# Performance work log

Measured on AMD Instinct MI355X. Metric: run time of the kernel, lower is better.

The kernel has to match this reference:

```python
import jax, jax.numpy as jnp
import numpy as np

N = 33554432  # 32M elements, 128 MB fp32

def setup_inputs() -> dict:
    key = jax.random.key(0)
    inp = jax.random.uniform(key, (N,), dtype=jnp.float32)
    return {"inp": inp}

def reference(inp) -> jnp.ndarray:
    # Faithful to the original: exp(x) / sum(exp(inp)) with NO max-subtraction
    # (the torch module computes the unstabilized softmax).
    e = jnp.exp(inp)
    return e / jnp.sum(e)
```

## Files before the change

### kernel.cpp

```cpp
#include <hip/hip_runtime.h>


#define BLOCK 256
#define RGRID 2048
#define SGRID 2048

typedef float vfloat4 __attribute__((ext_vector_type(4)));

__global__ __launch_bounds__(BLOCK) void softmax_reduce(
    const float* __restrict__ inp, float* __restrict__ partials, int n4) {
  const vfloat4* __restrict__ in4 = (const vfloat4*)inp;
  int tid = blockIdx.x * BLOCK + threadIdx.x;
  int stride = gridDim.x * BLOCK;

  float s0 = 0.0f, s1 = 0.0f;
  int i = tid;
  for (; i + stride < n4; i += 2 * stride) {
    vfloat4 a = in4[i];
    vfloat4 b = in4[i + stride];
    s0 += __expf(a.x) + __expf(a.y) + __expf(a.z) + __expf(a.w);
    s1 += __expf(b.x) + __expf(b.y) + __expf(b.z) + __expf(b.w);
  }
  for (; i < n4; i += stride) {
    vfloat4 a = in4[i];
    s0 += __expf(a.x) + __expf(a.y) + __expf(a.z) + __expf(a.w);
  }
  float s = s0 + s1;

  #pragma unroll
  for (int off = 32; off > 0; off >>= 1)
    s += __shfl_down(s, off, 64);

  __shared__ float wsum[BLOCK / 64];
  if ((threadIdx.x & 63) == 0) wsum[threadIdx.x >> 6] = s;
  __syncthreads();
  if (threadIdx.x == 0)
    partials[blockIdx.x] = wsum[0] + wsum[1] + wsum[2] + wsum[3];
}

__global__ __launch_bounds__(BLOCK) void softmax_scale(
    const float* __restrict__ inp, float* __restrict__ out,
    const float* __restrict__ partials, int n4) {
  float t = 0.0f;
  #pragma unroll
  for (int i = 0; i < RGRID / BLOCK; ++i)
    t += partials[i * BLOCK + threadIdx.x];

  #pragma unroll
  for (int off = 32; off > 0; off >>= 1)
    t += __shfl_down(t, off, 64);

  __shared__ float wsum[BLOCK / 64];
  if ((threadIdx.x & 63) == 0) wsum[threadIdx.x >> 6] = t;
  __syncthreads();
  float r = 1.0f / (wsum[0] + wsum[1] + wsum[2] + wsum[3]);

  const vfloat4* __restrict__ in4 = (const vfloat4*)inp;
  vfloat4* __restrict__ out4 = (vfloat4*)out;
  int tid = blockIdx.x * BLOCK + threadIdx.x;
  int stride = gridDim.x * BLOCK;

  int i = tid;
  for (; i + stride < n4; i += 2 * stride) {
    vfloat4 a = in4[i];
    vfloat4 b = in4[i + stride];
    vfloat4 oa, ob;
    oa.x = __expf(a.x) * r; oa.y = __expf(a.y) * r;
    oa.z = __expf(a.z) * r; oa.w = __expf(a.w) * r;
    ob.x = __expf(b.x) * r; ob.y = __expf(b.y) * r;
    ob.z = __expf(b.z) * r; ob.w = __expf(b.w) * r;
    __builtin_nontemporal_store(oa, &out4[i]);
    __builtin_nontemporal_store(ob, &out4[i + stride]);
  }
  for (; i < n4; i += stride) {
    vfloat4 a = in4[i];
    vfloat4 oa;
    oa.x = __expf(a.x) * r; oa.y = __expf(a.y) * r;
    oa.z = __expf(a.z) * r; oa.w = __expf(a.w) * r;
    __builtin_nontemporal_store(oa, &out4[i]);
  }
}

extern "C" void kernel_launch(void* const* d_in, const int* in_sizes, int n_in,
                              void* d_out, int out_size, void* d_ws, size_t ws_size,
                              hipStream_t stream) {
  const float* inp = (const float*)d_in[0];
  float* out = (float*)d_out;
  float* partials = (float*)d_ws;
  int n = in_sizes[0];
  int n4 = n >> 2;

  softmax_reduce<<<RGRID, BLOCK, 0, stream>>>(inp, partials, n4);
  softmax_scale<<<SGRID, BLOCK, 0, stream>>>(inp, out, partials, n4);
}
```

Baseline: 246.6 us.

## Store exp values in first pass and rescale output in place

The first kernel now writes exp(x) to the output buffer while accumulating partial sums, and reads the input with nontemporal loads. The second kernel reads that stored buffer back and multiplies by the reciprocal of the total, instead of re-reading the input and recomputing exp. This removes the second round of exp work, but it raises memory traffic from two reads and one write to two reads and two writes of the full array. Whether it pays off depends on the output buffer staying cached between the two passes.

```diff
diff --git a/kernel.cpp b/kernel.cpp
--- a/kernel.cpp
+++ b/kernel.cpp
@@ -2,28 +2,40 @@
 
 
 #define BLOCK 256
-#define RGRID 2048
-#define SGRID 2048
+#define GRID 2048
 
 typedef float vfloat4 __attribute__((ext_vector_type(4)));
 
-__global__ __launch_bounds__(BLOCK) void softmax_reduce(
-    const float* __restrict__ inp, float* __restrict__ partials, int n4) {
+__global__ __launch_bounds__(BLOCK) void softmax_pass1(
+    const float* __restrict__ inp, float* __restrict__ out,
+    float* __restrict__ partials, int n4) {
   const vfloat4* __restrict__ in4 = (const vfloat4*)inp;
-  int tid = blockIdx.x * BLOCK + threadIdx.x;
-  int stride = gridDim.x * BLOCK;
+  vfloat4* __restrict__ out4 = (vfloat4*)out;
+  const int tid = blockIdx.x * BLOCK + threadIdx.x;
+  const int stride = GRID * BLOCK;
 
   float s0 = 0.0f, s1 = 0.0f;
   int i = tid;
   for (; i + stride < n4; i += 2 * stride) {
-    vfloat4 a = in4[i];
-    vfloat4 b = in4[i + stride];
-    s0 += __expf(a.x) + __expf(a.y) + __expf(a.z) + __expf(a.w);
-    s1 += __expf(b.x) + __expf(b.y) + __expf(b.z) + __expf(b.w);
+    vfloat4 a = __builtin_nontemporal_load(&in4[i]);
+    vfloat4 b = __builtin_nontemporal_load(&in4[i + stride]);
+    vfloat4 ea, eb;
+    ea.x = __expf(a.x); ea.y = __expf(a.y);
+    ea.z = __expf(a.z); ea.w = __expf(a.w);
+    eb.x = __expf(b.x); eb.y = __expf(b.y);
+    eb.z = __expf(b.z); eb.w = __expf(b.w);
+    out4[i] = ea;
+    out4[i + stride] = eb;
+    s0 += ea.x + ea.y + ea.z + ea.w;
+    s1 += eb.x + eb.y + eb.z + eb.w;
   }
   for (; i < n4; i += stride) {
-    vfloat4 a = in4[i];
-    s0 += __expf(a.x) + __expf(a.y) + __expf(a.z) + __expf(a.w);
+    vfloat4 a = __builtin_nontemporal_load(&in4[i]);
+    vfloat4 ea;
+    ea.x = __expf(a.x); ea.y = __expf(a.y);
+    ea.z = __expf(a.z); ea.w = __expf(a.w);
+    out4[i] = ea;
+    s0 += ea.x + ea.y + ea.z + ea.w;
   }
   float s = s0 + s1;
 
@@ -38,13 +50,12 @@
     partials[blockIdx.x] = wsum[0] + wsum[1] + wsum[2] + wsum[3];
 }
 
-__global__ __launch_bounds__(BLOCK) void softmax_scale(
-    const float* __restrict__ inp, float* __restrict__ out,
-    const float* __restrict__ partials, int n4) {
+__global__ __launch_bounds__(BLOCK) void softmax_pass2(
+    float* __restrict__ out, const float* __restrict__ partials, int n4) {
   float t = 0.0f;
   #pragma unroll
-  for (int i = 0; i < RGRID / BLOCK; ++i)
-    t += partials[i * BLOCK + threadIdx.x];
+  for (int k = 0; k < GRID / BLOCK; ++k)
+    t += partials[k * BLOCK + threadIdx.x];
 
   #pragma unroll
   for (int off = 32; off > 0; off >>= 1)
@@ -53,31 +64,25 @@
   __shared__ float wsum[BLOCK / 64];
   if ((threadIdx.x & 63) == 0) wsum[threadIdx.x >> 6] = t;
   __syncthreads();
-  float r = 1.0f / (wsum[0] + wsum[1] + wsum[2] + wsum[3]);
+  const float r = 1.0f / (wsum[0] + wsum[1] + wsum[2] + wsum[3]);
 
-  const vfloat4* __restrict__ in4 = (const vfloat4*)inp;
   vfloat4* __restrict__ out4 = (vfloat4*)out;
-  int tid = blockIdx.x * BLOCK + threadIdx.x;
-  int stride = gridDim.x * BLOCK;
+  const int tid = blockIdx.x * BLOCK + threadIdx.x;
+  const int stride = GRID * BLOCK;
 
   int i = tid;
   for (; i + stride < n4; i += 2 * stride) {
-    vfloat4 a = in4[i];
-    vfloat4 b = in4[i + stride];
-    vfloat4 oa, ob;
-    oa.x = __expf(a.x) * r; oa.y = __expf(a.y) * r;
-    oa.z = __expf(a.z) * r; oa.w = __expf(a.w) * r;
-    ob.x = __expf(b.x) * r; ob.y = __expf(b.y) * r;
-    ob.z = __expf(b.z) * r; ob.w = __expf(b.w) * r;
-    __builtin_nontemporal_store(oa, &out4[i]);
-    __builtin_nontemporal_store(ob, &out4[i + stride]);
+    vfloat4 a = out4[i];
+    vfloat4 b = out4[i + stride];
+    a.x *= r; a.y *= r; a.z *= r; a.w *= r;
+    b.x *= r; b.y *= r; b.z *= r; b.w *= r;
+    out4[i] = a;
+    out4[i + stride] = b;
   }
   for (; i < n4; i += stride) {
-    vfloat4 a = in4[i];
-    vfloat4 oa;
-    oa.x = __expf(a.x) * r; oa.y = __expf(a.y) * r;
-    oa.z = __expf(a.z) * r; oa.w = __expf(a.w) * r;
-    __builtin_nontemporal_store(oa, &out4[i]);
+    vfloat4 a = out4[i];
+    a.x *= r; a.y *= r; a.z *= r; a.w *= r;
+    out4[i] = a;
   }
 }
 
@@ -90,6 +95,6 @@
   int n = in_sizes[0];
   int n4 = n >> 2;
 
-  softmax_reduce<<<RGRID, BLOCK, 0, stream>>>(inp, partials, n4);
-  softmax_scale<<<SGRID, BLOCK, 0, stream>>>(inp, out, partials, n4);
+  softmax_pass1<<<GRID, BLOCK, 0, stream>>>(inp, out, partials, n4);
+  softmax_pass2<<<GRID, BLOCK, 0, stream>>>(out, partials, n4);
 }
```

Measured after the change: 255.1 us. +3.5%, slower.
